# Kernel optimization log

Measured on AMD Instinct MI355X. Metric: run time of the kernel, lower is better.

Reference implementation:

```python
import jax, jax.numpy as jnp
import numpy as np

B = 1024          # batch of subject-object pairs
D_IN_HALF = 2048  # sbj/obj feature width; cat -> input_len = 4096
D_OUT = 1024      # output_len (embedding / label-vec width)
N_LABELS = 128    # number of relation labels in codebook


def setup_inputs() -> dict:
    key = jax.random.key(0)
    ks = jax.random.split(key, 7)
    s = 0.02  # small init scale for weights
    return {
        "sbj_vec": jax.random.normal(ks[0], (B, D_IN_HALF), jnp.float32),
        "obj_vec": jax.random.normal(ks[1], (B, D_IN_HALF), jnp.float32),
        "W1": jax.random.normal(ks[2], (2 * D_IN_HALF, D_OUT), jnp.float32) * s,
        "b1": jax.random.normal(ks[3], (D_OUT,), jnp.float32) * s,
        "W2": jax.random.normal(ks[4], (D_OUT, D_OUT), jnp.float32) * s,
        "b2": jax.random.normal(ks[5], (D_OUT,), jnp.float32) * s,
        "label_vecs": jax.random.normal(ks[6], (N_LABELS, D_OUT), jnp.float32),
    }


def reference(sbj_vec, obj_vec, W1, b1, W2, b2, label_vecs):
    # Sequential(ReLU, Dropout(eval=identity), Linear) applied twice.
    x = jnp.concatenate([sbj_vec, obj_vec], axis=1)          # [B, 2*D_IN_HALF]
    hidden = jax.nn.relu(x) @ W1 + b1                        # [B, D_OUT]
    emb = jax.nn.relu(hidden) @ W2 + b2                      # [B, D_OUT]
    # order_sim vs every label vector, fully batched (replaces per-sample loop):
    # sim[b, l] = -|| relu(label_vecs[l] - emb[b]) ||_2
    diff = jax.nn.relu(label_vecs[None, :, :] - emb[:, None, :])  # [B, L, D_OUT]
    scores = -jnp.sqrt(jnp.sum(diff * diff, axis=2))              # [B, L]
    return scores
```

## Files before the change

kernel.cpp:

```cpp
#include <hip/hip_runtime.h>
#include <math.h>

constexpr int Bn = 1024, DH = 2048, K1 = 4096, DO = 1024, NL = 128;
constexpr int MN = Bn * DO;

typedef __bf16 bf16x8 __attribute__((ext_vector_type(8)));
typedef short  s16x8  __attribute__((ext_vector_type(8)));
typedef float  f32x4  __attribute__((ext_vector_type(4)));

__device__ __forceinline__ unsigned short f2bf(float f) {
  union { float f; unsigned u; } v; v.f = f;
  unsigned r = v.u + 0x7FFFu + ((v.u >> 16) & 1u);
  return (unsigned short)(r >> 16);
}
__device__ __forceinline__ float bf2f(unsigned h) {
  union { unsigned u; float f; } v; v.u = h << 16; return v.f;
}

__global__ __launch_bounds__(256)
void prep(const float* __restrict__ sbj, const float* __restrict__ obj,
          const float* __restrict__ W1, const float* __restrict__ W2,
          unsigned short* __restrict__ Abf,
          unsigned short* __restrict__ W1t, unsigned short* __restrict__ W2t) {
  const int tid = threadIdx.x;
  if (blockIdx.x < 2048) {
    const int t = blockIdx.x * 256 + tid;
    const int m = t >> 9;
    const int k = (t & 511) << 3;
    const float* src = (k < DH) ? sbj + (size_t)m * DH + k
                                : obj + (size_t)m * DH + (k - DH);
    const float4 a = ((const float4*)src)[0];
    const float4 b = ((const float4*)src)[1];
    uint4 o;
    o.x = (unsigned)f2bf(fmaxf(a.x, 0.f)) | ((unsigned)f2bf(fmaxf(a.y, 0.f)) << 16);
    o.y = (unsigned)f2bf(fmaxf(a.z, 0.f)) | ((unsigned)f2bf(fmaxf(a.w, 0.f)) << 16);
    o.z = (unsigned)f2bf(fmaxf(b.x, 0.f)) | ((unsigned)f2bf(fmaxf(b.y, 0.f)) << 16);
    o.w = (unsigned)f2bf(fmaxf(b.z, 0.f)) | ((unsigned)f2bf(fmaxf(b.w, 0.f)) << 16);
    *(uint4*)&Abf[(size_t)m * K1 + k] = o;
    return;
  }
  __shared__ float tl[64][65];
  const int tb = blockIdx.x - 2048;
  int by = tb >> 4;
  const int c0 = (tb & 15) * 64;
  const float* in; unsigned short* out; int R;
  if (by < 64) { in = W1; out = W1t; R = K1; }
  else         { in = W2; out = W2t; R = DO; by -= 64; }
  const int r0 = by * 64;
  {
    const int rr = tid >> 4, cc = (tid & 15) * 4;
    #pragma unroll
    for (int i = 0; i < 4; ++i) {
      const float4 v = *(const float4*)&in[(size_t)(r0 + rr + i * 16) * DO + c0 + cc];
      tl[rr + i * 16][cc + 0] = v.x; tl[rr + i * 16][cc + 1] = v.y;
      tl[rr + i * 16][cc + 2] = v.z; tl[rr + i * 16][cc + 3] = v.w;
    }
  }
  __syncthreads();
  {
    const int r4 = (tid & 15) * 4;
    #pragma unroll
    for (int i = 0; i < 4; ++i) {
      const int cr = i * 16 + (tid >> 4);
      uint2 o;
      o.x = (unsigned)f2bf(tl[r4 + 0][cr]) | ((unsigned)f2bf(tl[r4 + 1][cr]) << 16);
      o.y = (unsigned)f2bf(tl[r4 + 2][cr]) | ((unsigned)f2bf(tl[r4 + 3][cr]) << 16);
      *(uint2*)&out[(size_t)(c0 + cr) * R + r0 + r4] = o;
    }
  }
}

template <int KSLICE>
__global__ __launch_bounds__(256, 2)
void mfma_gemm(const unsigned short* __restrict__ A,
               const unsigned short* __restrict__ Bt,
               unsigned short* __restrict__ P, int K) {
  __shared__ __align__(16) unsigned short smem[2 * 128 * 64];
  unsigned short* LA = smem;
  unsigned short* LB = smem + 128 * 64;

  const int tid = threadIdx.x;
  const int w = tid >> 6, l = tid & 63;
  const int bid = blockIdx.x;
  const int z = bid & 7, t = bid >> 3;
  const int m0 = (t >> 3) * 128, n0 = (t & 7) * 128;
  const int kb = z * KSLICE;

  f32x4 acc[4][4] = {};

  constexpr int NIT = KSLICE / 64;
  for (int it = 0; it < NIT; ++it) {
    const int k0 = kb + it * 64;
    #pragma unroll
    for (int i = 0; i < 4; ++i) {
      const int c = i * 256 + tid, row = c >> 3, kc = c & 7;
      const int kcg = kc ^ (row & 7);
      __builtin_amdgcn_global_load_lds(
          (const __attribute__((address_space(1))) unsigned int*)(A + (size_t)(m0 + row) * K + k0 + kcg * 8),
          (__attribute__((address_space(3))) unsigned int*)&LA[c * 8], 16, 0, 0);
    }
    #pragma unroll
    for (int i = 0; i < 4; ++i) {
      const int c = i * 256 + tid, row = c >> 3, kc = c & 7;
      const int kcg = kc ^ (row & 7);
      __builtin_amdgcn_global_load_lds(
          (const __attribute__((address_space(1))) unsigned int*)(Bt + (size_t)(n0 + row) * K + k0 + kcg * 8),
          (__attribute__((address_space(3))) unsigned int*)&LB[c * 8], 16, 0, 0);
    }
    __syncthreads();

    #pragma unroll
    for (int s = 0; s < 2; ++s) {
      const int kcq = s * 4 + (l >> 4);
      bf16x8 af[4], bfr[4];
      #pragma unroll
      for (int i = 0; i < 4; ++i) {
        const int r = (w >> 1) * 64 + i * 16 + (l & 15);
        const int kca = kcq ^ (r & 7);
        af[i] = __builtin_bit_cast(bf16x8, *(const s16x8*)&LA[(r * 8 + kca) * 8]);
      }
      #pragma unroll
      for (int j = 0; j < 4; ++j) {
        const int rr = (w & 1) * 64 + j * 16 + (l & 15);
        const int kcb = kcq ^ (rr & 7);
        bfr[j] = __builtin_bit_cast(bf16x8, *(const s16x8*)&LB[(rr * 8 + kcb) * 8]);
      }
      #pragma unroll
      for (int i = 0; i < 4; ++i)
        #pragma unroll
        for (int j = 0; j < 4; ++j)
          acc[i][j] = __builtin_amdgcn_mfma_f32_16x16x32_bf16(af[i], bfr[j], acc[i][j], 0, 0, 0);
    }
    __syncthreads();
  }

  unsigned short* Pz = P + (size_t)z * MN;
  #pragma unroll
  for (int i = 0; i < 4; ++i) {
    #pragma unroll
    for (int r = 0; r < 4; ++r) {
      const int m = m0 + (w >> 1) * 64 + i * 16 + (l >> 4) * 4 + r;
      #pragma unroll
      for (int j = 0; j < 4; ++j) {
        const int n = n0 + (w & 1) * 64 + j * 16 + (l & 15);
        Pz[(size_t)m * DO + n] = f2bf(acc[i][j][r]);
      }
    }
  }
}

__global__ __launch_bounds__(256)
void combine1(const unsigned short* __restrict__ P, const float* __restrict__ bias,
              unsigned short* __restrict__ out) {
  const int row = blockIdx.x, t = threadIdx.x;
  const size_t base = (size_t)row * DO + t * 4;
  float s0 = 0.f, s1 = 0.f, s2 = 0.f, s3 = 0.f;
  #pragma unroll
  for (int c = 0; c < 8; ++c) {
    const uint2 wv = *(const uint2*)&P[(size_t)c * MN + base];
    s0 += bf2f(wv.x & 0xFFFFu); s1 += bf2f(wv.x >> 16);
    s2 += bf2f(wv.y & 0xFFFFu); s3 += bf2f(wv.y >> 16);
  }
  const f32x4 bb = *(const f32x4*)&bias[t * 4];
  s0 = fmaxf(s0 + bb[0], 0.f); s1 = fmaxf(s1 + bb[1], 0.f);
  s2 = fmaxf(s2 + bb[2], 0.f); s3 = fmaxf(s3 + bb[3], 0.f);
  uint2 o;
  o.x = (unsigned)f2bf(s0) | ((unsigned)f2bf(s1) << 16);
  o.y = (unsigned)f2bf(s2) | ((unsigned)f2bf(s3) << 16);
  *(uint2*)&out[base] = o;
}

__global__ __launch_bounds__(256, 4)
void gemm2_full(const unsigned short* __restrict__ A,
                const unsigned short* __restrict__ Bt,
                const float* __restrict__ b2, float* __restrict__ E) {
  __shared__ __align__(16) unsigned short smem[2 * 64 * 128];
  unsigned short* LA = smem;
  unsigned short* LB = smem + 64 * 128;

  const int tid = threadIdx.x;
  const int w = tid >> 6, l = tid & 63;
  const int bid = blockIdx.x;
  const int m0 = (bid >> 4) * 64, n0 = (bid & 15) * 64;

  f32x4 acc[4][4] = {};

  for (int it = 0; it < 8; ++it) {
    const int k0 = it * 128;
    #pragma unroll
    for (int i = 0; i < 4; ++i) {
      const int c = i * 256 + tid, m = c >> 4, kc = c & 15;
      const int kcg = (kc & 8) | ((kc & 7) ^ (m & 7));
      __builtin_amdgcn_global_load_lds(
          (const __attribute__((address_space(1))) unsigned int*)(A + (size_t)(m0 + m) * DO + k0 + kcg * 8),
          (__attribute__((address_space(3))) unsigned int*)&LA[c * 8], 16, 0, 0);
    }
    #pragma unroll
    for (int i = 0; i < 4; ++i) {
      const int c = i * 256 + tid, n = c >> 4, kc = c & 15;
      const int kcg = (kc & 8) | ((kc & 7) ^ (n & 7));
      __builtin_amdgcn_global_load_lds(
          (const __attribute__((address_space(1))) unsigned int*)(Bt + (size_t)(n0 + n) * DO + k0 + kcg * 8),
          (__attribute__((address_space(3))) unsigned int*)&LB[c * 8], 16, 0, 0);
    }
    __syncthreads();

    const int kcq = w * 4 + (l >> 4);
    bf16x8 af[4], bfr[4];
    #pragma unroll
    for (int i = 0; i < 4; ++i) {
      const int r = i * 16 + (l & 15);
      const int kca = (kcq & 8) | ((kcq & 7) ^ (r & 7));
      af[i]  = __builtin_bit_cast(bf16x8, *(const s16x8*)&LA[(r * 16 + kca) * 8]);
      bfr[i] = __builtin_bit_cast(bf16x8, *(const s16x8*)&LB[(r * 16 + kca) * 8]);
    }
    #pragma unroll
    for (int i = 0; i < 4; ++i)
      #pragma unroll
      for (int j = 0; j < 4; ++j)
        acc[i][j] = __builtin_amdgcn_mfma_f32_16x16x32_bf16(af[i], bfr[j], acc[i][j], 0, 0, 0);
    __syncthreads();
  }

  float* red = (float*)smem;
  if (w >= 2) {
    #pragma unroll
    for (int i = 0; i < 4; ++i)
      #pragma unroll
      for (int j = 0; j < 4; ++j)
        *(f32x4*)&red[(w - 2) * 4096 + ((i * 4 + j) * 64 + l) * 4] = acc[i][j];
  }
  __syncthreads();
  if (w < 2) {
    #pragma unroll
    for (int i = 0; i < 4; ++i)
      #pragma unroll
      for (int j = 0; j < 4; ++j)
        acc[i][j] += *(const f32x4*)&red[w * 4096 + ((i * 4 + j) * 64 + l) * 4];
  }
  __syncthreads();
  if (w == 1) {
    #pragma unroll
    for (int i = 0; i < 2; ++i)
      #pragma unroll
      for (int j = 0; j < 4; ++j)
        *(f32x4*)&red[((i * 4 + j) * 64 + l) * 4] = acc[i][j];
  } else if (w == 0) {
    #pragma unroll
    for (int i = 0; i < 2; ++i)
      #pragma unroll
      for (int j = 0; j < 4; ++j)
        *(f32x4*)&red[2048 + ((i * 4 + j) * 64 + l) * 4] = acc[i + 2][j];
  }
  __syncthreads();
  if (w >= 2) return;

  if (w == 0) {
    #pragma unroll
    for (int i = 0; i < 2; ++i) {
      #pragma unroll
      for (int j = 0; j < 4; ++j)
        acc[i][j] += *(const f32x4*)&red[((i * 4 + j) * 64 + l) * 4];
      #pragma unroll
      for (int r = 0; r < 4; ++r) {
        const int m = m0 + i * 16 + (l >> 4) * 4 + r;
        #pragma unroll
        for (int j = 0; j < 4; ++j) {
          const int n = n0 + j * 16 + (l & 15);
          E[(size_t)m * DO + n] = acc[i][j][r] + b2[n];
        }
      }
    }
  } else {
    #pragma unroll
    for (int i = 0; i < 2; ++i) {
      #pragma unroll
      for (int j = 0; j < 4; ++j)
        acc[i + 2][j] += *(const f32x4*)&red[2048 + ((i * 4 + j) * 64 + l) * 4];
      #pragma unroll
      for (int r = 0; r < 4; ++r) {
        const int m = m0 + (i + 2) * 16 + (l >> 4) * 4 + r;
        #pragma unroll
        for (int j = 0; j < 4; ++j) {
          const int n = n0 + j * 16 + (l & 15);
          E[(size_t)m * DO + n] = acc[i + 2][j][r] + b2[n];
        }
      }
    }
  }
}

__global__ __launch_bounds__(256)
void score_partial(const float* __restrict__ E, const float* __restrict__ labels,
                   float* __restrict__ SP) {
  __shared__ float es[64][33];
  __shared__ float ls[64][132];
  const int tid = threadIdx.x;
  const int b0 = blockIdx.x * 32;
  const int d0 = blockIdx.y * 64;

  #pragma unroll
  for (int i = 0; i < 2; ++i) {
    const int fi = tid + i * 256;
    const int b = fi >> 4, dq = fi & 15;
    const float4 v = *(const float4*)&E[(size_t)(b0 + b) * DO + d0 + dq * 4];
    es[dq * 4 + 0][b] = v.x; es[dq * 4 + 1][b] = v.y;
    es[dq * 4 + 2][b] = v.z; es[dq * 4 + 3][b] = v.w;
  }
  #pragma unroll
  for (int i = 0; i < 8; ++i) {
    const int fi = tid + i * 256;
    const int lr = fi >> 4, dq = fi & 15;
    const float4 v = *(const float4*)&labels[(size_t)lr * DO + d0 + dq * 4];
    ls[dq * 4 + 0][lr] = v.x; ls[dq * 4 + 1][lr] = v.y;
    ls[dq * 4 + 2][lr] = v.z; ls[dq * 4 + 3][lr] = v.w;
  }
  __syncthreads();

  const int tb = tid & 15;
  const int tl = tid >> 4;
  float acc[2][8] = {};

  for (int dd = 0; dd < 64; ++dd) {
    const float e0 = es[dd][tb * 2 + 0];
    const float e1 = es[dd][tb * 2 + 1];
    const float4 l0 = *(const float4*)&ls[dd][tl * 8];
    const float4 l1 = *(const float4*)&ls[dd][tl * 8 + 4];
    const float lv[8] = {l0.x, l0.y, l0.z, l0.w, l1.x, l1.y, l1.z, l1.w};
    #pragma unroll
    for (int j = 0; j < 8; ++j) {
      float t0 = fmaxf(lv[j] - e0, 0.f); acc[0][j] = fmaf(t0, t0, acc[0][j]);
      float t1 = fmaxf(lv[j] - e1, 0.f); acc[1][j] = fmaf(t1, t1, acc[1][j]);
    }
  }

  float* SPz = SP + (size_t)blockIdx.y * (Bn * NL);
  #pragma unroll
  for (int i = 0; i < 2; ++i) {
    const size_t base = (size_t)(b0 + tb * 2 + i) * NL + tl * 8;
    float4 v0 = {acc[i][0], acc[i][1], acc[i][2], acc[i][3]};
    float4 v1 = {acc[i][4], acc[i][5], acc[i][6], acc[i][7]};
    *(float4*)&SPz[base]     = v0;
    *(float4*)&SPz[base + 4] = v1;
  }
}

__global__ __launch_bounds__(256)
void score_reduce(const float* __restrict__ SP, float* __restrict__ out) {
  const size_t i4 = (size_t)blockIdx.x * 256 + threadIdx.x;
  f32x4 s = ((const f32x4*)SP)[i4];
  #pragma unroll
  for (int c = 1; c < 16; ++c) s += ((const f32x4*)SP)[(size_t)c * 32768 + i4];
  f32x4 o = {-sqrtf(s[0]), -sqrtf(s[1]), -sqrtf(s[2]), -sqrtf(s[3])};
  ((f32x4*)out)[i4] = o;
}

extern "C" void kernel_launch(void* const* d_in, const int* in_sizes, int n_in,
                              void* d_out, int out_size, void* d_ws, size_t ws_size,
                              hipStream_t stream) {
  const float* sbj  = (const float*)d_in[0];
  const float* obj  = (const float*)d_in[1];
  const float* W1   = (const float*)d_in[2];
  const float* b1   = (const float*)d_in[3];
  const float* W2   = (const float*)d_in[4];
  const float* b2   = (const float*)d_in[5];
  const float* labs = (const float*)d_in[6];
  float* scores = (float*)d_out;
  char* ws = (char*)d_ws;

  unsigned short* Abf = (unsigned short*)(ws);
  unsigned short* W1t = (unsigned short*)(ws + (8ull << 20));
  unsigned short* W2t = (unsigned short*)(ws + (16ull << 20));
  unsigned short* H   = (unsigned short*)(ws + (18ull << 20));
  float* E  = (float*)(ws + (20ull << 20));
  unsigned short* P = (unsigned short*)(ws + (24ull << 20));
  float* SP = (float*)(ws + (40ull << 20));

  dim3 blk(256);
  prep<<<dim3(2048 + 1280), blk, 0, stream>>>(sbj, obj, W1, W2, Abf, W1t, W2t);

  mfma_gemm<512><<<dim3(512), blk, 0, stream>>>(Abf, W1t, P, K1);
  combine1<<<dim3(Bn), blk, 0, stream>>>(P, b1, H);
  gemm2_full<<<dim3(256), blk, 0, stream>>>(H, W2t, b2, E);
  score_partial<<<dim3(32, 16), blk, 0, stream>>>(E, labs, SP);
  score_reduce<<<dim3(128), blk, 0, stream>>>(SP, scores);
}
```

Baseline: 133.5 us.

## Double-buffer LDS in both GEMMs and halve score K-split partials

Both MFMA GEMM kernels now keep two LDS buffers and issue the async global→LDS loads for the next K tile before computing the current one. This removes one barrier per iteration and is meant to overlap memory latency with MFMA work. Separately, score_partial handles two 64-wide D chunks per block, which halves the partial-sum buffers that score_reduce must read. The cost is double the LDS footprint, which lowers occupancy (gemm2 launch bounds drop from 4 to 2 blocks per CU), and half as many score blocks.

```diff
diff --git a/kernel.cpp b/kernel.cpp
--- a/kernel.cpp
+++ b/kernel.cpp
@@ -75,9 +75,7 @@
 void mfma_gemm(const unsigned short* __restrict__ A,
                const unsigned short* __restrict__ Bt,
                unsigned short* __restrict__ P, int K) {
-  __shared__ __align__(16) unsigned short smem[2 * 128 * 64];
-  unsigned short* LA = smem;
-  unsigned short* LB = smem + 128 * 64;
+  __shared__ __align__(16) unsigned short smem[2][2 * 128 * 64];
 
   const int tid = threadIdx.x;
   const int w = tid >> 6, l = tid & 63;
@@ -89,8 +87,11 @@
   f32x4 acc[4][4] = {};
 
   constexpr int NIT = KSLICE / 64;
-  for (int it = 0; it < NIT; ++it) {
+
+  auto stage = [&](int buf, int it) {
     const int k0 = kb + it * 64;
+    unsigned short* LA = smem[buf];
+    unsigned short* LB = smem[buf] + 128 * 64;
     #pragma unroll
     for (int i = 0; i < 4; ++i) {
       const int c = i * 256 + tid, row = c >> 3, kc = c & 7;
@@ -107,8 +108,16 @@
           (const __attribute__((address_space(1))) unsigned int*)(Bt + (size_t)(n0 + row) * K + k0 + kcg * 8),
           (__attribute__((address_space(3))) unsigned int*)&LB[c * 8], 16, 0, 0);
     }
+  };
+
+  stage(0, 0);
+  int cur = 0;
+  for (int it = 0; it < NIT; ++it) {
     __syncthreads();
-
+    if (it + 1 < NIT) stage(cur ^ 1, it + 1);
+
+    const unsigned short* LA = smem[cur];
+    const unsigned short* LB = smem[cur] + 128 * 64;
     #pragma unroll
     for (int s = 0; s < 2; ++s) {
       const int kcq = s * 4 + (l >> 4);
@@ -131,7 +140,7 @@
         for (int j = 0; j < 4; ++j)
           acc[i][j] = __builtin_amdgcn_mfma_f32_16x16x32_bf16(af[i], bfr[j], acc[i][j], 0, 0, 0);
     }
-    __syncthreads();
+    cur ^= 1;
   }
 
   unsigned short* Pz = P + (size_t)z * MN;
@@ -170,13 +179,11 @@
   *(uint2*)&out[base] = o;
 }
 
-__global__ __launch_bounds__(256, 4)
+__global__ __launch_bounds__(256, 2)
 void gemm2_full(const unsigned short* __restrict__ A,
                 const unsigned short* __restrict__ Bt,
                 const float* __restrict__ b2, float* __restrict__ E) {
-  __shared__ __align__(16) unsigned short smem[2 * 64 * 128];
-  unsigned short* LA = smem;
-  unsigned short* LB = smem + 64 * 128;
+  __shared__ __align__(16) unsigned short smem[2][2 * 64 * 128];
 
   const int tid = threadIdx.x;
   const int w = tid >> 6, l = tid & 63;
@@ -185,8 +192,10 @@
 
   f32x4 acc[4][4] = {};
 
-  for (int it = 0; it < 8; ++it) {
+  auto stage = [&](int buf, int it) {
     const int k0 = it * 128;
+    unsigned short* LA = smem[buf];
+    unsigned short* LB = smem[buf] + 64 * 128;
     #pragma unroll
     for (int i = 0; i < 4; ++i) {
       const int c = i * 256 + tid, m = c >> 4, kc = c & 15;
@@ -203,8 +212,16 @@
           (const __attribute__((address_space(1))) unsigned int*)(Bt + (size_t)(n0 + n) * DO + k0 + kcg * 8),
           (__attribute__((address_space(3))) unsigned int*)&LB[c * 8], 16, 0, 0);
     }
+  };
+
+  stage(0, 0);
+  int cur = 0;
+  for (int it = 0; it < 8; ++it) {
     __syncthreads();
-
+    if (it + 1 < 8) stage(cur ^ 1, it + 1);
+
+    const unsigned short* LA = smem[cur];
+    const unsigned short* LB = smem[cur] + 64 * 128;
     const int kcq = w * 4 + (l >> 4);
     bf16x8 af[4], bfr[4];
     #pragma unroll
@@ -219,8 +236,9 @@
       #pragma unroll
       for (int j = 0; j < 4; ++j)
         acc[i][j] = __builtin_amdgcn_mfma_f32_16x16x32_bf16(af[i], bfr[j], acc[i][j], 0, 0, 0);
-    __syncthreads();
-  }
+    cur ^= 1;
+  }
+  __syncthreads();
 
   float* red = (float*)smem;
   if (w >= 2) {
@@ -297,40 +315,45 @@
   __shared__ float ls[64][132];
   const int tid = threadIdx.x;
   const int b0 = blockIdx.x * 32;
-  const int d0 = blockIdx.y * 64;
-
-  #pragma unroll
-  for (int i = 0; i < 2; ++i) {
-    const int fi = tid + i * 256;
-    const int b = fi >> 4, dq = fi & 15;
-    const float4 v = *(const float4*)&E[(size_t)(b0 + b) * DO + d0 + dq * 4];
-    es[dq * 4 + 0][b] = v.x; es[dq * 4 + 1][b] = v.y;
-    es[dq * 4 + 2][b] = v.z; es[dq * 4 + 3][b] = v.w;
-  }
-  #pragma unroll
-  for (int i = 0; i < 8; ++i) {
-    const int fi = tid + i * 256;
-    const int lr = fi >> 4, dq = fi & 15;
-    const float4 v = *(const float4*)&labels[(size_t)lr * DO + d0 + dq * 4];
-    ls[dq * 4 + 0][lr] = v.x; ls[dq * 4 + 1][lr] = v.y;
-    ls[dq * 4 + 2][lr] = v.z; ls[dq * 4 + 3][lr] = v.w;
-  }
-  __syncthreads();
 
   const int tb = tid & 15;
   const int tl = tid >> 4;
   float acc[2][8] = {};
 
-  for (int dd = 0; dd < 64; ++dd) {
-    const float e0 = es[dd][tb * 2 + 0];
-    const float e1 = es[dd][tb * 2 + 1];
-    const float4 l0 = *(const float4*)&ls[dd][tl * 8];
-    const float4 l1 = *(const float4*)&ls[dd][tl * 8 + 4];
-    const float lv[8] = {l0.x, l0.y, l0.z, l0.w, l1.x, l1.y, l1.z, l1.w};
-    #pragma unroll
-    for (int j = 0; j < 8; ++j) {
-      float t0 = fmaxf(lv[j] - e0, 0.f); acc[0][j] = fmaf(t0, t0, acc[0][j]);
-      float t1 = fmaxf(lv[j] - e1, 0.f); acc[1][j] = fmaf(t1, t1, acc[1][j]);
+  #pragma unroll
+  for (int ch = 0; ch < 2; ++ch) {
+    const int d0 = blockIdx.y * 128 + ch * 64;
+    if (ch) __syncthreads();
+
+    #pragma unroll
+    for (int i = 0; i < 2; ++i) {
+      const int fi = tid + i * 256;
+      const int b = fi >> 4, dq = fi & 15;
+      const float4 v = *(const float4*)&E[(size_t)(b0 + b) * DO + d0 + dq * 4];
+      es[dq * 4 + 0][b] = v.x; es[dq * 4 + 1][b] = v.y;
+      es[dq * 4 + 2][b] = v.z; es[dq * 4 + 3][b] = v.w;
+    }
+    #pragma unroll
+    for (int i = 0; i < 8; ++i) {
+      const int fi = tid + i * 256;
+      const int lr = fi >> 4, dq = fi & 15;
+      const float4 v = *(const float4*)&labels[(size_t)lr * DO + d0 + dq * 4];
+      ls[dq * 4 + 0][lr] = v.x; ls[dq * 4 + 1][lr] = v.y;
+      ls[dq * 4 + 2][lr] = v.z; ls[dq * 4 + 3][lr] = v.w;
+    }
+    __syncthreads();
+
+    for (int dd = 0; dd < 64; ++dd) {
+      const float e0 = es[dd][tb * 2 + 0];
+      const float e1 = es[dd][tb * 2 + 1];
+      const float4 l0 = *(const float4*)&ls[dd][tl * 8];
+      const float4 l1 = *(const float4*)&ls[dd][tl * 8 + 4];
+      const float lv[8] = {l0.x, l0.y, l0.z, l0.w, l1.x, l1.y, l1.z, l1.w};
+      #pragma unroll
+      for (int j = 0; j < 8; ++j) {
+        float t0 = fmaxf(lv[j] - e0, 0.f); acc[0][j] = fmaf(t0, t0, acc[0][j]);
+        float t1 = fmaxf(lv[j] - e1, 0.f); acc[1][j] = fmaf(t1, t1, acc[1][j]);
+      }
     }
   }
 
@@ -350,7 +373,7 @@
   const size_t i4 = (size_t)blockIdx.x * 256 + threadIdx.x;
   f32x4 s = ((const f32x4*)SP)[i4];
   #pragma unroll
-  for (int c = 1; c < 16; ++c) s += ((const f32x4*)SP)[(size_t)c * 32768 + i4];
+  for (int c = 1; c < 8; ++c) s += ((const f32x4*)SP)[(size_t)c * 32768 + i4];
   f32x4 o = {-sqrtf(s[0]), -sqrtf(s[1]), -sqrtf(s[2]), -sqrtf(s[3])};
   ((f32x4*)out)[i4] = o;
 }
@@ -382,6 +405,6 @@
   mfma_gemm<512><<<dim3(512), blk, 0, stream>>>(Abf, W1t, P, K1);
   combine1<<<dim3(Bn), blk, 0, stream>>>(P, b1, H);
   gemm2_full<<<dim3(256), blk, 0, stream>>>(H, W2t, b2, E);
-  score_partial<<<dim3(32, 16), blk, 0, stream>>>(E, labs, SP);
+  score_partial<<<dim3(32, 8), blk, 0, stream>>>(E, labs, SP);
   score_reduce<<<dim3(128), blk, 0, stream>>>(SP, scores);
 }
```

Result: no change. 133.6 us (+0.0%).
